# Kernel optimization log

Measured on AMD Instinct MI355X. Metric: run time of the kernel, lower is better.

## Reference

```python
import jax, jax.numpy as jnp
import numpy as np

B, T, H = 8, 4096, 512
K = 8192  # codebook size


def setup_inputs() -> dict:
    key = jax.random.key(0)
    kz, ke = jax.random.split(key)
    z = jax.random.normal(kz, (B, T, H), dtype=jnp.float32)
    emb = jax.random.normal(ke, (K, H), dtype=jnp.float32) * 0.02
    return {"z": z, "emb": emb}


def reference(z, emb):
    b, t, h = z.shape
    flat = z.reshape(b * t, h)
    dist = (jnp.sum(flat * flat, axis=1, keepdims=True)
            - 2.0 * (flat @ emb.T)
            + jnp.sum(emb * emb, axis=1)[None, :])
    idx = jnp.argmin(dist, axis=1)            # (b*t,)
    z_q = emb[idx].reshape(b, t, h)           # codebook lookup
    # straight-through estimator
    z_st = z + jax.lax.stop_gradient(z_q - z)
    codebook_loss = jnp.mean((z_q - jax.lax.stop_gradient(z)) ** 2)
    commit_loss = jnp.mean((z - jax.lax.stop_gradient(z_q)) ** 2)
    return z_st, idx.reshape(b, t), codebook_loss, commit_loss
```

## Files before the change

kernel.cpp:

```cpp
#include <hip/hip_runtime.h>
#include <cstdint>
#include <cstddef>

#define M_ROWS 32768
#define K_CODES 8192
#define H_DIM 512
#define TAU 2.5e-4f
#define MAXFLAG 32768

typedef float  f32x4 __attribute__((ext_vector_type(4)));
typedef short  s16x8 __attribute__((ext_vector_type(8)));

typedef __attribute__((address_space(3))) void as3_void;
typedef const __attribute__((address_space(1))) void as1_cvoid;
#define GLD16(gp, lp) __builtin_amdgcn_global_load_lds((as1_cvoid*)(gp), (as3_void*)(lp), 16, 0, 0)

__device__ __forceinline__ unsigned short f2bf(float f) {
    uint32_t u = __float_as_uint(f);
    u = u + 0x7fffu + ((u >> 16) & 1u);
    return (unsigned short)(u >> 16);
}
__device__ __forceinline__ float bf2f(unsigned short h) {
    return __uint_as_float(((uint32_t)h) << 16);
}

__device__ __forceinline__ float np_sumsq_row32(const float* row, int lane32) {
    const int c = lane32 >> 3, j = lane32 & 7;
    const float* p = row + c * 128 + j;
    float s = __fmul_rn(p[0], p[0]);
    #pragma unroll
    for (int t = 1; t < 16; ++t) {
        const float v = p[8 * t];
        s = __fadd_rn(s, __fmul_rn(v, v));
    }
    s = __fadd_rn(s, __shfl_xor(s, 1));
    s = __fadd_rn(s, __shfl_xor(s, 2));
    s = __fadd_rn(s, __shfl_xor(s, 4));
    s = __fadd_rn(s, __shfl_xor(s, 8));
    s = __fadd_rn(s, __shfl_xor(s, 16));
    return s;
}

__global__ __launch_bounds__(256) void prep_kernel(
    const float* __restrict__ z, const float* __restrict__ emb,
    unsigned short* __restrict__ zh, unsigned short* __restrict__ zl,
    unsigned short* __restrict__ eh, unsigned short* __restrict__ el,
    float* __restrict__ x2, float* __restrict__ e2,
    float* __restrict__ loss_slots, int* __restrict__ flag_count, int do_split)
{
    __shared__ float zr[8][512];
    const int row0 = blockIdx.x * 8;

    #pragma unroll
    for (int k = 0; k < 4; ++k) {
        const int f  = threadIdx.x + k * 256;
        const int r  = f >> 7;
        const int c4 = f & 127;
        const int grow = row0 + r;
        const float* src; unsigned short* hi; unsigned short* lo; size_t off;
        if (grow < M_ROWS) { src = z;   hi = zh; lo = zl; off = (size_t)grow * H_DIM; }
        else               { src = emb; hi = eh; lo = el; off = (size_t)(grow - M_ROWS) * H_DIM; }
        const float4 v = *reinterpret_cast<const float4*>(src + off + (size_t)c4 * 4);
        zr[r][c4 * 4 + 0] = v.x;
        zr[r][c4 * 4 + 1] = v.y;
        zr[r][c4 * 4 + 2] = v.z;
        zr[r][c4 * 4 + 3] = v.w;
        if (do_split) {
            ushort4 h, l;
            h.x = f2bf(v.x); l.x = f2bf(v.x - bf2f(h.x));
            h.y = f2bf(v.y); l.y = f2bf(v.y - bf2f(h.y));
            h.z = f2bf(v.z); l.z = f2bf(v.z - bf2f(h.z));
            h.w = f2bf(v.w); l.w = f2bf(v.w - bf2f(h.w));
            *reinterpret_cast<ushort4*>(hi + off + (size_t)c4 * 4) = h;
            *reinterpret_cast<ushort4*>(lo + off + (size_t)c4 * 4) = l;
        }
    }
    __syncthreads();

    const int r = threadIdx.x >> 5;
    const float s = np_sumsq_row32(&zr[r][0], threadIdx.x & 31);
    if ((threadIdx.x & 31) == 0) {
        const int grow = row0 + r;
        if (grow < M_ROWS) x2[grow] = s;
        else               e2[grow - M_ROWS] = s;
    }
    if (blockIdx.x == 0) {
        if (threadIdx.x < 2) loss_slots[threadIdx.x] = 0.f;
        if (threadIdx.x == 0) *flag_count = 0;
    }
}

__device__ __forceinline__ void top2_merge(float& b1, int& ix, float& b2,
                                           float ob1, int oix, float ob2) {
    if (ob1 < b1)      { b2 = fminf(b1, ob2); b1 = ob1; ix = oix; }
    else if (ob1 > b1) { b2 = fminf(b2, ob1); }
    else               { if (oix < ix) ix = oix; b2 = b1; }
}

__global__ __launch_bounds__(512, 1) void mfma_dist_kernel(
    const unsigned short* __restrict__ zh, const unsigned short* __restrict__ zl,
    const unsigned short* __restrict__ eh, const unsigned short* __restrict__ el,
    const float* __restrict__ x2, const float* __restrict__ e2,
    float* __restrict__ pb1, float* __restrict__ pb2, int* __restrict__ pidx)
{
    __shared__ __align__(16) unsigned short lb[2][4][8192];

    const int tid = threadIdx.x;
    const int l   = tid & 63;
    const int w   = tid >> 6;
    const int wm  = w >> 2;
    const int wn  = w & 3;

    const int bid  = blockIdx.x;
    const int xcd  = bid & 7;
    const int sq   = bid >> 3;
    const int band = sq >> 7;
    const int r128 = sq & 127;
    const int ct   = r128 >> 2;
    const int rt   = (band * 8 + xcd) * 4 + (r128 & 3);
    const int row0 = rt * 256;
    const int c0   = ct * 256;

    const int m    = w >> 1;
    const int half = w & 1;
    const unsigned short* sp = (m == 0) ? zh : (m == 1) ? zl : (m == 2) ? eh : el;
    const int rbase0 = (m < 2) ? row0 : c0;
    const unsigned short* sb = sp
        + (size_t)(rbase0 + half * 128 + (l >> 2)) * H_DIM
        + ((l & 3) ^ ((l >> 3) & 3)) * 8;

    const int aoff = (wm * 128 + (l & 15)) * 64 + (((l >> 4) ^ ((l >> 1) & 3)) * 16);
    const int boff = (wn * 64  + (l & 15)) * 64 + (((l >> 4) ^ ((l >> 1) & 3)) * 16);

    f32x4 acc[8][4];
    #pragma unroll
    for (int i = 0; i < 8; ++i)
        #pragma unroll
        for (int j = 0; j < 4; ++j)
            acc[i][j] = (f32x4){0.f, 0.f, 0.f, 0.f};

    {
        char* dst = (char*)&lb[0][m][0] + half * 8192;
        #pragma unroll
        for (int t = 0; t < 8; ++t)
            GLD16(sb + (size_t)t * 16 * H_DIM, dst + t * 1024);
    }
    asm volatile("s_waitcnt vmcnt(0)" ::: "memory");
    __builtin_amdgcn_s_barrier();

#define MFMA_PAIR(I0, AH0, AV0, AH1, AV1)                                                        \
    _Pragma("unroll")                                                                            \
    for (int j = 0; j < 4; ++j) {                                                                \
        acc[I0][j]     = __builtin_amdgcn_mfma_f32_16x16x32_bf16(AV0, bh[j], acc[I0][j], 0,0,0); \
        acc[I0][j]     = __builtin_amdgcn_mfma_f32_16x16x32_bf16(AH0, bv[j], acc[I0][j], 0,0,0); \
        acc[I0][j]     = __builtin_amdgcn_mfma_f32_16x16x32_bf16(AH0, bh[j], acc[I0][j], 0,0,0); \
        acc[I0+1][j]   = __builtin_amdgcn_mfma_f32_16x16x32_bf16(AV1, bh[j], acc[I0+1][j], 0,0,0); \
        acc[I0+1][j]   = __builtin_amdgcn_mfma_f32_16x16x32_bf16(AH1, bv[j], acc[I0+1][j], 0,0,0); \
        acc[I0+1][j]   = __builtin_amdgcn_mfma_f32_16x16x32_bf16(AH1, bh[j], acc[I0+1][j], 0,0,0); \
    }

    for (int s = 0; s < 16; ++s) {
        const int par = s & 1;
        const char* pAh = (const char*)&lb[par][0][0];
        const char* pAl = (const char*)&lb[par][1][0];
        const char* pBh = (const char*)&lb[par][2][0];
        const char* pBl = (const char*)&lb[par][3][0];
        char* dst = (char*)&lb[par ^ 1][m][0] + half * 8192;
        const unsigned short* src = sb + (s + 1) * 32;
        const bool pf = (s < 15);

        s16x8 bh[4], bv[4];

        {
            #pragma unroll
            for (int j = 0; j < 4; ++j) {
                bh[j] = *(const s16x8*)(pBh + boff + j * 1024);
                bv[j] = *(const s16x8*)(pBl + boff + j * 1024);
            }
            const s16x8 a0h = *(const s16x8*)(pAh + aoff + 0 * 1024);
            const s16x8 a0v = *(const s16x8*)(pAl + aoff + 0 * 1024);
            const s16x8 a1h = *(const s16x8*)(pAh + aoff + 1 * 1024);
            const s16x8 a1v = *(const s16x8*)(pAl + aoff + 1 * 1024);
            if (pf) {
                GLD16(src + (size_t)0 * 16 * H_DIM, dst + 0 * 1024);
                GLD16(src + (size_t)1 * 16 * H_DIM, dst + 1 * 1024);
                GLD16(src + (size_t)2 * 16 * H_DIM, dst + 2 * 1024);
                GLD16(src + (size_t)3 * 16 * H_DIM, dst + 3 * 1024);
            }
            __builtin_amdgcn_sched_barrier(0);
            __builtin_amdgcn_s_barrier();
            asm volatile("s_waitcnt lgkmcnt(0)" ::: "memory");
            __builtin_amdgcn_sched_barrier(0);
            __builtin_amdgcn_s_setprio(1);
            MFMA_PAIR(0, a0h, a0v, a1h, a1v)
            __builtin_amdgcn_s_setprio(0);
            __builtin_amdgcn_s_barrier();
        }
        {
            const s16x8 a0h = *(const s16x8*)(pAh + aoff + 2 * 1024);
            const s16x8 a0v = *(const s16x8*)(pAl + aoff + 2 * 1024);
            const s16x8 a1h = *(const s16x8*)(pAh + aoff + 3 * 1024);
            const s16x8 a1v = *(const s16x8*)(pAl + aoff + 3 * 1024);
            if (pf) {
                GLD16(src + (size_t)4 * 16 * H_DIM, dst + 4 * 1024);
                GLD16(src + (size_t)5 * 16 * H_DIM, dst + 5 * 1024);
                GLD16(src + (size_t)6 * 16 * H_DIM, dst + 6 * 1024);
                GLD16(src + (size_t)7 * 16 * H_DIM, dst + 7 * 1024);
            }
            __builtin_amdgcn_sched_barrier(0);
            __builtin_amdgcn_s_barrier();
            asm volatile("s_waitcnt lgkmcnt(0)" ::: "memory");
            __builtin_amdgcn_sched_barrier(0);
            __builtin_amdgcn_s_setprio(1);
            MFMA_PAIR(2, a0h, a0v, a1h, a1v)
            __builtin_amdgcn_s_setprio(0);
            __builtin_amdgcn_s_barrier();
        }
        {
            const s16x8 a0h = *(const s16x8*)(pAh + aoff + 4 * 1024);
            const s16x8 a0v = *(const s16x8*)(pAl + aoff + 4 * 1024);
            const s16x8 a1h = *(const s16x8*)(pAh + aoff + 5 * 1024);
            const s16x8 a1v = *(const s16x8*)(pAl + aoff + 5 * 1024);
            __builtin_amdgcn_sched_barrier(0);
            __builtin_amdgcn_s_barrier();
            asm volatile("s_waitcnt lgkmcnt(0)" ::: "memory");
            __builtin_amdgcn_sched_barrier(0);
            __builtin_amdgcn_s_setprio(1);
            MFMA_PAIR(4, a0h, a0v, a1h, a1v)
            __builtin_amdgcn_s_setprio(0);
            __builtin_amdgcn_s_barrier();
        }
        {
            const s16x8 a0h = *(const s16x8*)(pAh + aoff + 6 * 1024);
            const s16x8 a0v = *(const s16x8*)(pAl + aoff + 6 * 1024);
            const s16x8 a1h = *(const s16x8*)(pAh + aoff + 7 * 1024);
            const s16x8 a1v = *(const s16x8*)(pAl + aoff + 7 * 1024);
            __builtin_amdgcn_sched_barrier(0);
            __builtin_amdgcn_s_barrier();
            asm volatile("s_waitcnt lgkmcnt(0)" ::: "memory");
            __builtin_amdgcn_sched_barrier(0);
            __builtin_amdgcn_s_setprio(1);
            MFMA_PAIR(6, a0h, a0v, a1h, a1v)
            __builtin_amdgcn_s_setprio(0);
            asm volatile("s_waitcnt vmcnt(0)" ::: "memory");
            __builtin_amdgcn_s_barrier();
        }
    }
#undef MFMA_PAIR

    float* mb1 = (float*)&lb[0][0][0];
    float* mb2 = mb1 + 1024;
    int*   mi  = (int*)(mb1 + 2048);

    float e2v[4];
    #pragma unroll
    for (int j = 0; j < 4; ++j)
        e2v[j] = e2[c0 + wn * 64 + j * 16 + (l & 15)];

    #pragma unroll
    for (int i = 0; i < 8; ++i) {
        const float4 x2v = *reinterpret_cast<const float4*>(
            x2 + row0 + wm * 128 + i * 16 + (l >> 4) * 4);
        const float x2a[4] = {x2v.x, x2v.y, x2v.z, x2v.w};
        #pragma unroll
        for (int r = 0; r < 4; ++r) {
            float b1 = 3.4e38f, b2 = 3.4e38f; int ix = 0;
            #pragma unroll
            for (int j = 0; j < 4; ++j) {
                const float d = __fadd_rn(__fmaf_rn(-2.f, acc[i][j][r], x2a[r]), e2v[j]);
                const int cj = c0 + wn * 64 + j * 16 + (l & 15);
                if (d < b1)      { b2 = b1; b1 = d; ix = cj; }
                else if (d < b2) { b2 = d; }
            }
            #pragma unroll
            for (int mm = 1; mm <= 8; mm <<= 1) {
                const float ob1 = __shfl_xor(b1, mm);
                const float ob2 = __shfl_xor(b2, mm);
                const int   oix = __shfl_xor(ix, mm);
                top2_merge(b1, ix, b2, ob1, oix, ob2);
            }
            if ((l & 15) == 0) {
                const int rl = wm * 128 + i * 16 + (l >> 4) * 4 + r;
                mb1[wn * 256 + rl] = b1;
                mb2[wn * 256 + rl] = b2;
                mi [wn * 256 + rl] = ix;
            }
        }
    }
    __syncthreads();
    if (tid < 256) {
        float b1 = mb1[tid], b2 = mb2[tid]; int ix = mi[tid];
        #pragma unroll
        for (int q = 1; q < 4; ++q)
            top2_merge(b1, ix, b2, mb1[q * 256 + tid], mi[q * 256 + tid], mb2[q * 256 + tid]);
        const size_t o = (size_t)ct * M_ROWS + row0 + tid;
        pb1[o] = b1; pb2[o] = b2; pidx[o] = ix;
    }
}

__global__ __launch_bounds__(256) void combine_kernel(
    const float* __restrict__ pb1, const float* __restrict__ pb2,
    const int* __restrict__ pidx,
    int* __restrict__ idx_i, float* __restrict__ idx_f,
    int* __restrict__ flag_count, int* __restrict__ flag_rows)
{
    const int r = blockIdx.x * 256 + threadIdx.x;
    if (r >= M_ROWS) return;
    float b1 = pb1[r], b2 = pb2[r]; int ix = pidx[r];
    #pragma unroll 4
    for (int ct = 1; ct < 32; ++ct)
        top2_merge(b1, ix, b2, pb1[(size_t)ct * M_ROWS + r],
                   pidx[(size_t)ct * M_ROWS + r], pb2[(size_t)ct * M_ROWS + r]);
    idx_i[r] = ix;
    idx_f[r] = (float)ix;
    if (b2 - b1 < TAU) {
        const int p = atomicAdd(flag_count, 1);
        if (p < MAXFLAG) flag_rows[p] = r;
    }
}

#define BM 64
#define BN 128
#define BH 32
#define PADZ 4
#define PADE 4

__device__ __forceinline__ void stage_transposed(const float* __restrict__ src,
                                                 int row0, int h0,
                                                 float* lds, int R, int ldp) {
    const int nf4 = R * (BH / 4);
    for (int f = threadIdx.x; f < nf4; f += 256) {
        const int r  = f / (BH / 4);
        const int c4 = (f % (BH / 4)) * 4;
        const float4 v = *reinterpret_cast<const float4*>(
            src + (size_t)(row0 + r) * H_DIM + h0 + c4);
        lds[(c4 + 0) * ldp + r] = v.x;
        lds[(c4 + 1) * ldp + r] = v.y;
        lds[(c4 + 2) * ldp + r] = v.z;
        lds[(c4 + 3) * ldp + r] = v.w;
    }
}

__global__ __launch_bounds__(256) void dist_argmin_kernel(
    const float* __restrict__ z, const float* __restrict__ emb,
    const float* __restrict__ x2, const float* __restrict__ e2,
    int* __restrict__ idx_i, float* __restrict__ idx_f,
    int* __restrict__ flag_count, int* __restrict__ flag_rows)
{
    __shared__ float zs[BH * (BM + PADZ)];
    __shared__ float es[BH * (BN + PADE)];
    __shared__ float bd[BM][17];
    __shared__ float bd2[BM][17];
    __shared__ int   bi[BM][17];

    const int row0 = blockIdx.x * BM;
    const int tx = threadIdx.x & 15;
    const int ty = threadIdx.x >> 4;

    float x2r[4];
    #pragma unroll
    for (int i = 0; i < 4; ++i) x2r[i] = x2[row0 + ty * 4 + i];

    float best[4], best2[4];
    int   bidx[4];
    #pragma unroll
    for (int i = 0; i < 4; ++i) { best[i] = 3.4e38f; best2[i] = 3.4e38f; bidx[i] = 0; }

    for (int nt = 0; nt < K_CODES / BN; ++nt) {
        float acc[4][8];
        #pragma unroll
        for (int i = 0; i < 4; ++i)
            #pragma unroll
            for (int j = 0; j < 8; ++j) acc[i][j] = 0.f;

        for (int hc = 0; hc < H_DIM / BH; ++hc) {
            __syncthreads();
            stage_transposed(z,   row0,    hc * BH, zs, BM, BM + PADZ);
            stage_transposed(emb, nt * BN, hc * BH, es, BN, BN + PADE);
            __syncthreads();
            #pragma unroll
            for (int h = 0; h < BH; ++h) {
                const float4 zr = *reinterpret_cast<const float4*>(&zs[h * (BM + PADZ) + ty * 4]);
                const float4 e0 = *reinterpret_cast<const float4*>(&es[h * (BN + PADE) + tx * 4]);
                const float4 e1 = *reinterpret_cast<const float4*>(&es[h * (BN + PADE) + 64 + tx * 4]);
                const float zrv[4] = {zr.x, zr.y, zr.z, zr.w};
                const float ev[8]  = {e0.x, e0.y, e0.z, e0.w, e1.x, e1.y, e1.z, e1.w};
                #pragma unroll
                for (int i = 0; i < 4; ++i)
                    #pragma unroll
                    for (int j = 0; j < 8; ++j)
                        acc[i][j] = fmaf(zrv[i], ev[j], acc[i][j]);
            }
        }
        #pragma unroll
        for (int j = 0; j < 8; ++j) {
            const int code = nt * BN + (j < 4 ? tx * 4 + j : 64 + tx * 4 + (j - 4));
            const float e2v = e2[code];
            #pragma unroll
            for (int i = 0; i < 4; ++i) {
                const float d = __fadd_rn(__fmaf_rn(-2.f, acc[i][j], x2r[i]), e2v);
                if (d < best[i])       { best2[i] = best[i]; best[i] = d; bidx[i] = code; }
                else if (d < best2[i]) { best2[i] = d; }
            }
        }
    }

    __syncthreads();
    #pragma unroll
    for (int i = 0; i < 4; ++i) {
        bd [ty * 4 + i][tx] = best[i];
        bd2[ty * 4 + i][tx] = best2[i];
        bi [ty * 4 + i][tx] = bidx[i];
    }
    __syncthreads();
    if (threadIdx.x < BM) {
        const int r = threadIdx.x;
        float g1 = bd[r][0]; int gi = bi[r][0]; float g2 = bd2[r][0];
        #pragma unroll
        for (int t = 1; t < 16; ++t) {
            const float v = bd[r][t]; const int x = bi[r][t];
            if (v < g1)       { g2 = g1; g1 = v; gi = x; }
            else if (v == g1) { g2 = g1; if (x < gi) gi = x; }
            else              { g2 = fminf(g2, v); }
            g2 = fminf(g2, bd2[r][t]);
        }
        idx_i[row0 + r] = gi;
        idx_f[row0 + r] = (float)gi;
        if (g2 - g1 < TAU) {
            const int p = atomicAdd(flag_count, 1);
            if (p < MAXFLAG) flag_rows[p] = row0 + r;
        }
    }
}

__global__ __launch_bounds__(256) void fixup_scan_kernel(
    const float* __restrict__ z, const float* __restrict__ emb,
    const float* __restrict__ x2, const float* __restrict__ e2,
    const int* __restrict__ flag_count, const int* __restrict__ flag_rows,
    float* __restrict__ qb1, int* __restrict__ qix)
{
    __shared__ float zrow[H_DIM];
    __shared__ float sd[256];
    __shared__ int   si[256];
    int n = *flag_count; if (n > MAXFLAG) n = MAXFLAG;
    const int q = blockIdx.x & 3;
    for (int j = blockIdx.x >> 2; j < n; j += (gridDim.x >> 2)) {
        const int row = flag_rows[j];
        __syncthreads();
        for (int h = threadIdx.x; h < H_DIM; h += 256)
            zrow[h] = z[(size_t)row * H_DIM + h];
        __syncthreads();
        const float x2r = x2[row];
        float bdv = 3.4e38f; int biv = 0x7fffffff;
        for (int k = q * 2048 + threadIdx.x; k < q * 2048 + 2048; k += 256) {
            const float* ek = emb + (size_t)k * H_DIM;
            double d0 = 0.0, d1 = 0.0, d2 = 0.0, d3 = 0.0;
            for (int h = 0; h < H_DIM; h += 4) {
                const float4 ev = *reinterpret_cast<const float4*>(ek + h);
                const float4 zv = *reinterpret_cast<const float4*>(&zrow[h]);
                d0 = fma((double)zv.x, (double)ev.x, d0);
                d1 = fma((double)zv.y, (double)ev.y, d1);
                d2 = fma((double)zv.z, (double)ev.z, d2);
                d3 = fma((double)zv.w, (double)ev.w, d3);
            }
            const float gf = (float)((d0 + d1) + (d2 + d3));
            const float d = __fadd_rn(__fmaf_rn(-2.f, gf, x2r), e2[k]);
            if (d < bdv) { bdv = d; biv = k; }
        }
        sd[threadIdx.x] = bdv; si[threadIdx.x] = biv;
        __syncthreads();
        for (int s = 128; s; s >>= 1) {
            if (threadIdx.x < s) {
                const float od = sd[threadIdx.x + s]; const int oi = si[threadIdx.x + s];
                if (od < sd[threadIdx.x] ||
                    (od == sd[threadIdx.x] && oi < si[threadIdx.x])) {
                    sd[threadIdx.x] = od; si[threadIdx.x] = oi;
                }
            }
            __syncthreads();
        }
        if (threadIdx.x == 0) { qb1[j * 4 + q] = sd[0]; qix[j * 4 + q] = si[0]; }
        __syncthreads();
    }
}

__global__ __launch_bounds__(256) void fixup_merge_kernel(
    const int* __restrict__ flag_count, const int* __restrict__ flag_rows,
    const float* __restrict__ qb1, const int* __restrict__ qix,
    int* __restrict__ idx_i, float* __restrict__ idx_f)
{
    int n = *flag_count; if (n > MAXFLAG) n = MAXFLAG;
    const int t = blockIdx.x * 256 + threadIdx.x;
    if (t >= n) return;
    float b = qb1[t * 4]; int ix = qix[t * 4];
    #pragma unroll
    for (int q = 1; q < 4; ++q) {
        const float ob = qb1[t * 4 + q];
        if (ob < b) { b = ob; ix = qix[t * 4 + q]; }
    }
    idx_i[flag_rows[t]] = ix;
    idx_f[flag_rows[t]] = (float)ix;
}

__global__ __launch_bounds__(256) void epilogue_kernel(
    const float* __restrict__ z, const float* __restrict__ emb,
    const int* __restrict__ idx_i,
    float* __restrict__ z_st, float* __restrict__ loss_slots)
{
    const int NQ = M_ROWS * (H_DIM / 4);
    const float4* z4 = reinterpret_cast<const float4*>(z);
    const float4* e4 = reinterpret_cast<const float4*>(emb);
    float4* o4 = reinterpret_cast<float4*>(z_st);
    float local = 0.f;
    for (int q = blockIdx.x * 256 + threadIdx.x; q < NQ; q += gridDim.x * 256) {
        const int r  = q >> 7;
        const int h4 = q & 127;
        const float4 zq = e4[(size_t)idx_i[r] * 128 + h4];
        const float4 zv = z4[q];
        float4 t, o;
        t.x = zq.x - zv.x; o.x = zv.x + t.x;
        t.y = zq.y - zv.y; o.y = zv.y + t.y;
        t.z = zq.z - zv.z; o.z = zv.z + t.z;
        t.w = zq.w - zv.w; o.w = zv.w + t.w;
        o4[q] = o;
        local = fmaf(t.x, t.x, local);
        local = fmaf(t.y, t.y, local);
        local = fmaf(t.z, t.z, local);
        local = fmaf(t.w, t.w, local);
    }
    #pragma unroll
    for (int off = 32; off; off >>= 1) local += __shfl_down(local, off);
    __shared__ float part[4];
    const int lane = threadIdx.x & 63, wid = threadIdx.x >> 6;
    if (lane == 0) part[wid] = local;
    __syncthreads();
    if (threadIdx.x == 0) {
        const float s = (part[0] + part[1] + part[2] + part[3])
                        * (1.f / (float)((size_t)M_ROWS * H_DIM));
        atomicAdd(&loss_slots[0], s);
        atomicAdd(&loss_slots[1], s);
    }
}

extern "C" void kernel_launch(void* const* d_in, const int* in_sizes, int n_in,
                              void* d_out, int out_size, void* d_ws, size_t ws_size,
                              hipStream_t stream) {
    const float* z   = (const float*)d_in[0];
    const float* emb = (const float*)d_in[1];

    float* out   = (float*)d_out;
    float* z_st  = out;
    float* idx_f = out + (size_t)M_ROWS * H_DIM;
    float* loss  = out + (size_t)M_ROWS * H_DIM + M_ROWS;

    float* pb1  = z_st;
    float* pb2  = z_st + (size_t)32 * M_ROWS;
    int*   pidx = (int*)(z_st + (size_t)64 * M_ROWS);
    float* qb1  = z_st + (size_t)96 * M_ROWS;
    int*   qix  = (int*)(z_st + (size_t)96 * M_ROWS + 4 * MAXFLAG);

    char* ws = (char*)d_ws;
    float* e2     = (float*)(ws + 0);
    float* x2     = (float*)(ws + 32768);
    int*   idx_i  = (int*)  (ws + 163840);
    int*   fcount = (int*)  (ws + 294912);
    int*   frows  = (int*)  (ws + 294976);
    unsigned short* zh = (unsigned short*)(ws + 426048);
    unsigned short* zl = (unsigned short*)(ws + 426048 + 33554432ull);
    unsigned short* eh = (unsigned short*)(ws + 426048 + 67108864ull);
    unsigned short* el = (unsigned short*)(ws + 426048 + 75497472ull);
    const size_t REQ = 426048ull + 83886080ull;

    const int use_mfma = (ws_size >= REQ) ? 1 : 0;

    hipLaunchKernelGGL(prep_kernel, dim3((M_ROWS + K_CODES) / 8), dim3(256), 0, stream,
                       z, emb, zh, zl, eh, el, x2, e2, loss, fcount, use_mfma);

    if (use_mfma) {
        hipLaunchKernelGGL(mfma_dist_kernel, dim3(4096), dim3(512), 0, stream,
                           zh, zl, eh, el, x2, e2, pb1, pb2, pidx);
        hipLaunchKernelGGL(combine_kernel, dim3(M_ROWS / 256), dim3(256), 0, stream,
                           pb1, pb2, pidx, idx_i, idx_f, fcount, frows);
    } else {
        hipLaunchKernelGGL(dist_argmin_kernel, dim3(M_ROWS / BM), dim3(256), 0, stream,
                           z, emb, x2, e2, idx_i, idx_f, fcount, frows);
    }

    hipLaunchKernelGGL(fixup_scan_kernel, dim3(8192), dim3(256), 0, stream,
                       z, emb, x2, e2, fcount, frows, qb1, qix);
    hipLaunchKernelGGL(fixup_merge_kernel, dim3(MAXFLAG / 256), dim3(256), 0, stream,
                       fcount, frows, qb1, qix, idx_i, idx_f);
    hipLaunchKernelGGL(epilogue_kernel, dim3(2048), dim3(256), 0, stream,
                       z, emb, idx_i, z_st, loss);
}
```

Before: 1.142 ms.

## Prefilter fixup candidates with fp32 distance before fp64 rescoring; tighten flag threshold

Halves the near-tie flag threshold so fewer rows go to the exact fixup pass, and records each flagged row's best distance. The fixup scan now computes an fp32 distance per code first and skips the costly fp64 dot product unless it falls within a small margin of that best. The merge step also breaks equal-distance ties by lowest index. The risk is mis-resolved near ties if the fp32 prefilter or the tighter threshold drops the true argmin.

```diff
diff --git a/kernel.cpp b/kernel.cpp
--- a/kernel.cpp
+++ b/kernel.cpp
@@ -5,7 +5,8 @@
 #define M_ROWS 32768
 #define K_CODES 8192
 #define H_DIM 512
-#define TAU 2.5e-4f
+#define TAU 1.2e-4f
+#define CUTPAD 2.0e-4f
 #define MAXFLAG 32768
 
 typedef float  f32x4 __attribute__((ext_vector_type(4)));
@@ -302,7 +303,8 @@
     const float* __restrict__ pb1, const float* __restrict__ pb2,
     const int* __restrict__ pidx,
     int* __restrict__ idx_i, float* __restrict__ idx_f,
-    int* __restrict__ flag_count, int* __restrict__ flag_rows)
+    int* __restrict__ flag_count, int* __restrict__ flag_rows,
+    float* __restrict__ flag_b1)
 {
     const int r = blockIdx.x * 256 + threadIdx.x;
     if (r >= M_ROWS) return;
@@ -315,7 +317,7 @@
     idx_f[r] = (float)ix;
     if (b2 - b1 < TAU) {
         const int p = atomicAdd(flag_count, 1);
-        if (p < MAXFLAG) flag_rows[p] = r;
+        if (p < MAXFLAG) { flag_rows[p] = r; flag_b1[p] = b1; }
     }
 }
 
@@ -345,7 +347,8 @@
     const float* __restrict__ z, const float* __restrict__ emb,
     const float* __restrict__ x2, const float* __restrict__ e2,
     int* __restrict__ idx_i, float* __restrict__ idx_f,
-    int* __restrict__ flag_count, int* __restrict__ flag_rows)
+    int* __restrict__ flag_count, int* __restrict__ flag_rows,
+    float* __restrict__ flag_b1)
 {
     __shared__ float zs[BH * (BM + PADZ)];
     __shared__ float es[BH * (BN + PADE)];
@@ -428,7 +431,7 @@
         idx_f[row0 + r] = (float)gi;
         if (g2 - g1 < TAU) {
             const int p = atomicAdd(flag_count, 1);
-            if (p < MAXFLAG) flag_rows[p] = row0 + r;
+            if (p < MAXFLAG) { flag_rows[p] = row0 + r; flag_b1[p] = g1; }
         }
     }
 }
@@ -437,6 +440,7 @@
     const float* __restrict__ z, const float* __restrict__ emb,
     const float* __restrict__ x2, const float* __restrict__ e2,
     const int* __restrict__ flag_count, const int* __restrict__ flag_rows,
+    const float* __restrict__ flag_b1,
     float* __restrict__ qb1, int* __restrict__ qix)
 {
     __shared__ float zrow[H_DIM];
@@ -451,9 +455,22 @@
             zrow[h] = z[(size_t)row * H_DIM + h];
         __syncthreads();
         const float x2r = x2[row];
+        const float cut = flag_b1[j] + CUTPAD;
         float bdv = 3.4e38f; int biv = 0x7fffffff;
         for (int k = q * 2048 + threadIdx.x; k < q * 2048 + 2048; k += 256) {
             const float* ek = emb + (size_t)k * H_DIM;
+            float f0 = 0.f, f1 = 0.f, f2 = 0.f, f3 = 0.f;
+            for (int h = 0; h < H_DIM; h += 4) {
+                const float4 ev = *reinterpret_cast<const float4*>(ek + h);
+                const float4 zv = *reinterpret_cast<const float4*>(&zrow[h]);
+                f0 = fmaf(zv.x, ev.x, f0);
+                f1 = fmaf(zv.y, ev.y, f1);
+                f2 = fmaf(zv.z, ev.z, f2);
+                f3 = fmaf(zv.w, ev.w, f3);
+            }
+            const float g32 = (f0 + f1) + (f2 + f3);
+            const float d32 = __fadd_rn(__fmaf_rn(-2.f, g32, x2r), e2[k]);
+            if (d32 >= cut) continue;
             double d0 = 0.0, d1 = 0.0, d2 = 0.0, d3 = 0.0;
             for (int h = 0; h < H_DIM; h += 4) {
                 const float4 ev = *reinterpret_cast<const float4*>(ek + h);
@@ -496,7 +513,8 @@
     #pragma unroll
     for (int q = 1; q < 4; ++q) {
         const float ob = qb1[t * 4 + q];
-        if (ob < b) { b = ob; ix = qix[t * 4 + q]; }
+        const int   oi = qix[t * 4 + q];
+        if (ob < b || (ob == b && oi < ix)) { b = ob; ix = oi; }
     }
     idx_i[flag_rows[t]] = ix;
     idx_f[flag_rows[t]] = (float)ix;
@@ -558,6 +576,7 @@
     int*   pidx = (int*)(z_st + (size_t)64 * M_ROWS);
     float* qb1  = z_st + (size_t)96 * M_ROWS;
     int*   qix  = (int*)(z_st + (size_t)96 * M_ROWS + 4 * MAXFLAG);
+    float* fb1  = z_st + (size_t)96 * M_ROWS + 8 * MAXFLAG;
 
     char* ws = (char*)d_ws;
     float* e2     = (float*)(ws + 0);
@@ -580,14 +599,14 @@
         hipLaunchKernelGGL(mfma_dist_kernel, dim3(4096), dim3(512), 0, stream,
                            zh, zl, eh, el, x2, e2, pb1, pb2, pidx);
         hipLaunchKernelGGL(combine_kernel, dim3(M_ROWS / 256), dim3(256), 0, stream,
-                           pb1, pb2, pidx, idx_i, idx_f, fcount, frows);
+                           pb1, pb2, pidx, idx_i, idx_f, fcount, frows, fb1);
     } else {
         hipLaunchKernelGGL(dist_argmin_kernel, dim3(M_ROWS / BM), dim3(256), 0, stream,
-                           z, emb, x2, e2, idx_i, idx_f, fcount, frows);
+                           z, emb, x2, e2, idx_i, idx_f, fcount, frows, fb1);
     }
 
     hipLaunchKernelGGL(fixup_scan_kernel, dim3(8192), dim3(256), 0, stream,
-                       z, emb, x2, e2, fcount, frows, qb1, qix);
+                       z, emb, x2, e2, fcount, frows, fb1, qb1, qix);
     hipLaunchKernelGGL(fixup_merge_kernel, dim3(MAXFLAG / 256), dim3(256), 0, stream,
                        fcount, frows, qb1, qix, idx_i, idx_f);
     hipLaunchKernelGGL(epilogue_kernel, dim3(2048), dim3(256), 0, stream,
```

Measured after the change: 1.145 ms. No clear change (+0.2%).
